# Kernel optimization log

Measured on AMD Instinct MI355X. Metric: run time of the kernel, lower is better.

## Reference

```python
import jax, jax.numpy as jnp
import numpy as np

B_, L_, D_ = 2, 1024, 2048
E_, N_, R_, K_ = 4096, 16, 128, 4
EPS = 1e-5


def setup_inputs() -> dict:
    key = jax.random.key(0)
    ks = jax.random.split(key, 12)
    s = lambda i, shape, scale=0.02: jax.random.normal(ks[i], shape, jnp.float32) * scale
    # dt bias init as in the module: inv_dt = dt + log(-expm1(-dt)), dt ~ logU[1e-3, 0.1]
    dt = jnp.exp(jax.random.uniform(ks[10], (E_,)) * (np.log(0.1) - np.log(0.001)) + np.log(0.001))
    inv_dt = dt + jnp.log(-jnp.expm1(-dt))
    return {
        'resid': jax.random.normal(ks[0], (B_, L_, D_), jnp.float32),
        'norm_w': jnp.ones((D_,), jnp.float32),
        'skip_w': s(1, (E_, D_)),
        'in_w': s(2, (E_, D_)),
        'conv_w': s(3, (E_, K_), 0.2),
        'conv_b': jnp.zeros((E_,), jnp.float32),
        'wd1': s(4, (R_, E_)),
        'wd2': s(5, (E_, R_), R_ ** -0.5),
        'wd2_b': inv_dt,
        'wB': s(6, (N_, E_)),
        'wC': s(7, (N_, E_)),
        'A_log': jnp.log(jnp.broadcast_to(jnp.arange(1, N_ + 1, dtype=jnp.float32), (E_, N_))),
        'W_D': jnp.ones((E_,), jnp.float32),
        'out_w': s(8, (D_, E_)),
    }


def _forward(resid, norm_w, skip_w, in_w, conv_w, conv_b, wd1, wd2, wd2_b,
             wB, wC, A_log, W_D, out_w):
    B, L, D = resid.shape
    E, K = conv_w.shape
    N = A_log.shape[1]
    # RMSNorm
    rn = resid * jax.lax.rsqrt(jnp.mean(resid * resid, -1, keepdims=True) + EPS) * norm_w
    skip = rn @ skip_w.T                       # [B,L,E] gate branch (z)
    x_in = rn @ in_w.T                         # [B,L,E]
    # depthwise causal conv1d (pad left K-1, truncate to L), then SiLU
    xp = jnp.pad(x_in, ((0, 0), (K - 1, 0), (0, 0)))
    conv = conv_b + sum(xp[:, k:k + L, :] * conv_w[:, k] for k in range(K))
    x = jax.nn.silu(conv)                      # [B,L,E] ssm input
    # low-rank delta, input-dependent B/C
    delta = jax.nn.softplus((x @ wd1.T) @ wd2.T + wd2_b)   # [B,L,E]
    A = -jnp.exp(A_log)                        # [E,N]
    Bm = x @ wB.T                              # [B,L,N]
    Cm = x @ wC.T                              # [B,L,N]

    def step(h, inp):
        d_l, b_l, c_l, x_l = inp               # [B,E],[B,N],[B,N],[B,E]
        h = jnp.exp(d_l[:, :, None] * A) * h + (d_l * x_l)[:, :, None] * b_l[:, None, :]
        y_l = jnp.einsum('ben,bn->be', h, c_l)
        return h, y_l

    h0 = jnp.zeros((B, E, N), resid.dtype)
    xs = (delta.transpose(1, 0, 2), Bm.transpose(1, 0, 2),
          Cm.transpose(1, 0, 2), x.transpose(1, 0, 2))
    _, ys = jax.lax.scan(step, h0, xs)         # ys: [L,B,E]
    y = ys.transpose(1, 0, 2) + x * W_D        # skip connection via D
    y = y * jax.nn.silu(skip)                  # gating
    return resid + y @ out_w.T                 # out_proj + residual


def reference(resid, norm_w, skip_w, in_w, conv_w, conv_b, wd1, wd2, wd2_b,
              wB, wC, A_log, W_D, out_w):
    return _forward(resid, norm_w, skip_w, in_w, conv_w, conv_b, wd1, wd2,
                    wd2_b, wB, wC, A_log, W_D, out_w)
```

## Files before the change

### kernel.cpp

```cpp
#include <hip/hip_runtime.h>
#include <stdint.h>

#define NB 2
#define NL 1024
#define ND 2048
#define NE 4096
#define NN 16
#define NR 128
#define NKC 4
#define NBL (NB*NL)
#define EPSV 1e-5f

typedef __attribute__((ext_vector_type(4))) float f32x4;
typedef __attribute__((ext_vector_type(8))) short short8;
typedef __attribute__((ext_vector_type(8))) unsigned short ushort8;
typedef __attribute__((ext_vector_type(4))) unsigned short ushort4_t;

__device__ __forceinline__ unsigned short f2bf(float f) {
  union { float f; unsigned u; } v; v.f = f;
  unsigned r = v.u + 0x7FFFu + ((v.u >> 16) & 1u);
  return (unsigned short)(r >> 16);
}

__device__ __forceinline__ float bf2f(unsigned short u) {
  union { unsigned u; float f; } v; v.u = (unsigned)u << 16; return v.f;
}

__device__ __forceinline__ void load_lds16(const void* g, void* l) {
  __builtin_amdgcn_global_load_lds((const __attribute__((address_space(1))) void*)g,
                                   (__attribute__((address_space(3))) void*)l,
                                   16, 0, 0);
}

template<int CTRL>
__device__ __forceinline__ float dpp_mov(float v) {
  return __int_as_float(__builtin_amdgcn_update_dpp(
      0, __float_as_int(v), CTRL, 0xF, 0xF, true));
}

__global__ void rmsnorm_kernel(const float* __restrict__ resid,
                               const float* __restrict__ nw,
                               unsigned short* __restrict__ rn) {
  int row = blockIdx.x;
  int tid = threadIdx.x;
  const float* r = resid + (size_t)row * ND;
  f32x4 v0 = *(const f32x4*)(r + tid * 8);
  f32x4 v1 = *(const f32x4*)(r + tid * 8 + 4);
  float vals[8];
#pragma unroll
  for (int i = 0; i < 4; ++i) { vals[i] = v0[i]; vals[4 + i] = v1[i]; }
  float ss = 0.f;
#pragma unroll
  for (int i = 0; i < 8; ++i) ss += vals[i] * vals[i];
  for (int o = 32; o > 0; o >>= 1) ss += __shfl_down(ss, o);
  __shared__ float ps[4];
  if ((tid & 63) == 0) ps[tid >> 6] = ss;
  __syncthreads();
  float tot = ps[0] + ps[1] + ps[2] + ps[3];
  float scale = rsqrtf(tot / (float)ND + EPSV);
  ushort8 o8;
#pragma unroll
  for (int i = 0; i < 8; ++i) o8[i] = f2bf(vals[i] * scale * nw[tid * 8 + i]);
  *(ushort8*)(rn + (size_t)row * ND + tid * 8) = o8;
}

__global__ void cast_bf16_kernel(const float* __restrict__ in,
                                 unsigned short* __restrict__ out, int n8) {
  int i = blockIdx.x * blockDim.x + threadIdx.x;
  if (i >= n8) return;
  f32x4 a = *(const f32x4*)(in + (size_t)i * 8);
  f32x4 b = *(const f32x4*)(in + (size_t)i * 8 + 4);
  ushort8 o;
#pragma unroll
  for (int j = 0; j < 4; ++j) { o[j] = f2bf(a[j]); o[4 + j] = f2bf(b[j]); }
  *(ushort8*)(out + (size_t)i * 8) = o;
}

__global__ void build_wcat_kernel(const float* __restrict__ wd1,
                                  const float* __restrict__ wB,
                                  const float* __restrict__ wC,
                                  unsigned short* __restrict__ out) {
  int i = blockIdx.x * blockDim.x + threadIdx.x;
  if (i >= 256 * NE / 8) return;
  int col8 = i & (NE / 8 - 1);
  int row = i >> 9;
  const float* src = nullptr; int srow = 0;
  if (row < 128)      { src = wd1; srow = row; }
  else if (row < 144) { src = wB;  srow = row - 128; }
  else if (row < 160) { src = wC;  srow = row - 144; }
  ushort8 o;
  if (src) {
    f32x4 a = *(const f32x4*)(src + (size_t)srow * NE + col8 * 8);
    f32x4 b = *(const f32x4*)(src + (size_t)srow * NE + col8 * 8 + 4);
#pragma unroll
    for (int j = 0; j < 4; ++j) { o[j] = f2bf(a[j]); o[4 + j] = f2bf(b[j]); }
  } else {
#pragma unroll
    for (int j = 0; j < 8; ++j) o[j] = 0;
  }
  *(ushort8*)(out + (size_t)row * NE + col8 * 8) = o;
}

__global__ __launch_bounds__(512, 2)
void gemm256_fused(const unsigned short* __restrict__ A,
                   const unsigned short* __restrict__ B,
                   float* __restrict__ Gout,
                   unsigned short* __restrict__ Xout) {
  const int K = 2048, NH = K / 32;
  __shared__ unsigned short Asl[4][8192];
  __shared__ unsigned short Bsl[4][8192];
  int tid = threadIdx.x;
  int w = tid >> 6, lane = tid & 63;
  int wm = w >> 2, wn = w & 3;
  int lr = lane & 15, kg8 = (lane >> 4) * 8;
  int m0 = blockIdx.y * 256, n0 = blockIdx.x * 256;

  const unsigned short* ga = A + (size_t)(m0 + (tid >> 2)) * K + (tid & 3) * 8;
  const unsigned short* gb = B + (size_t)(n0 + (tid >> 2)) * K + (tid & 3) * 8;
  char* ldsA0 = (char*)&Asl[0][0] + w * 1024;
  char* ldsB0 = (char*)&Bsl[0][0] + w * 1024;

  auto stageA = [&](int h) {
    int slot = h & 3, k0 = h * 32;
    load_lds16(ga + k0, ldsA0 + slot * 16384);
    load_lds16(ga + k0 + (size_t)128 * K, ldsA0 + slot * 16384 + 8192);
  };
  auto stageB = [&](int h) {
    int slot = h & 3, k0 = h * 32;
    load_lds16(gb + k0, ldsB0 + slot * 16384);
    load_lds16(gb + k0 + (size_t)128 * K, ldsB0 + slot * 16384 + 8192);
  };

  f32x4 acc[8][4];
#pragma unroll
  for (int i = 0; i < 8; ++i)
#pragma unroll
    for (int j = 0; j < 4; ++j) acc[i][j] = (f32x4){0.f, 0.f, 0.f, 0.f};

  stageA(0); stageB(0); stageA(1); stageB(1); stageA(2); stageB(2);
  asm volatile("s_waitcnt vmcnt(8)" ::: "memory");
  __builtin_amdgcn_s_barrier();

  for (int h = 0; h < NH; ++h) {
    int slot = h & 3;
    const unsigned short* As_ = &Asl[slot][0];
    const unsigned short* Bs_ = &Bsl[slot][0];
    int arow = wm * 128 + lr;
    int brow = wn * 64 + lr;
    short8 a[8], b[4];
#pragma unroll
    for (int i = 0; i < 4; ++i)
      a[i] = *(const short8*)&As_[(arow + i * 16) * 32 + kg8];
#pragma unroll
    for (int j = 0; j < 4; ++j)
      b[j] = *(const short8*)&Bs_[(brow + j * 16) * 32 + kg8];
    if (h + 3 < NH) stageA(h + 3);
    __builtin_amdgcn_s_barrier();
    __builtin_amdgcn_s_setprio(1);
#pragma unroll
    for (int i = 0; i < 4; ++i)
#pragma unroll
      for (int j = 0; j < 4; ++j)
        acc[i][j] = __builtin_amdgcn_mfma_f32_16x16x32_bf16(a[i], b[j], acc[i][j], 0, 0, 0);
    __builtin_amdgcn_s_setprio(0);
    __builtin_amdgcn_s_barrier();
#pragma unroll
    for (int i = 0; i < 4; ++i)
      a[4 + i] = *(const short8*)&As_[(arow + (4 + i) * 16) * 32 + kg8];
    if (h + 3 < NH) stageB(h + 3);
    __builtin_amdgcn_s_barrier();
    __builtin_amdgcn_s_setprio(1);
#pragma unroll
    for (int i = 0; i < 4; ++i)
#pragma unroll
      for (int j = 0; j < 4; ++j)
        acc[4 + i][j] = __builtin_amdgcn_mfma_f32_16x16x32_bf16(a[4 + i], b[j], acc[4 + i][j], 0, 0, 0);
    __builtin_amdgcn_s_setprio(0);
    if (h < NH - 3)       { asm volatile("s_waitcnt vmcnt(8)" ::: "memory"); }
    else if (h == NH - 3) { asm volatile("s_waitcnt vmcnt(4)" ::: "memory"); }
    else if (h == NH - 2) { asm volatile("s_waitcnt vmcnt(0)" ::: "memory"); }
    __builtin_amdgcn_s_barrier();
  }

  int rbase = m0 + wm * 128 + (lane >> 4) * 4;
  int cbase = n0 + wn * 64 + (lane & 15);
  bool isg = (n0 < 4096);
#pragma unroll
  for (int mf = 0; mf < 8; ++mf) {
#pragma unroll
    for (int nf = 0; nf < 4; ++nf) {
      int col = cbase + nf * 16;
#pragma unroll
      for (int rr = 0; rr < 4; ++rr) {
        int row = rbase + mf * 16 + rr;
        float v = acc[mf][nf][rr];
        if (isg) Gout[(size_t)row * 4096 + col] = v / (1.f + __expf(-v));
        else     Xout[(size_t)row * 4096 + (col - 4096)] = f2bf(v);
      }
    }
  }
}

template<int MODE>
__global__ __launch_bounds__(256)
void gemm_bt(const unsigned short* __restrict__ A,
             const unsigned short* __restrict__ B,
             float* __restrict__ C,
             int M, int N, int K, int ksteps_per_z,
             const float* __restrict__ bias,
             const float* __restrict__ add) {
  __shared__ unsigned short As[128 * 32];
  __shared__ unsigned short Bs[128 * 32];
  int tid = threadIdx.x;
  int w = tid >> 6, lane = tid & 63;
  int m0 = blockIdx.y * 128, n0 = blockIdx.x * 128;
  int kz0 = blockIdx.z * ksteps_per_z * 32;
  if (MODE == 0) C += (size_t)blockIdx.z * M * N;

  f32x4 zero = {0.f, 0.f, 0.f, 0.f};
  f32x4 acc[4][4];
#pragma unroll
  for (int i = 0; i < 4; ++i)
#pragma unroll
    for (int j = 0; j < 4; ++j) acc[i][j] = zero;

  int wm = w >> 1, wn = w & 1;
  int lr = lane & 15, kg = lane >> 4;

  int fe0 = (w)*512 + lane * 8;
  int fe1 = (4 + w) * 512 + lane * 8;
  int r0 = fe0 >> 5, c0 = fe0 & 31;
  int r1 = fe1 >> 5, c1 = fe1 & 31;
  const unsigned short* Ag0 = A + (size_t)(m0 + r0) * K + c0;
  const unsigned short* Ag1 = A + (size_t)(m0 + r1) * K + c1;
  const unsigned short* Bg0 = B + (size_t)(n0 + r0) * K + c0;
  const unsigned short* Bg1 = B + (size_t)(n0 + r1) * K + c1;
  unsigned short* Al0 = As + (w) * 512;
  unsigned short* Al1 = As + (4 + w) * 512;
  unsigned short* Bl0 = Bs + (w) * 512;
  unsigned short* Bl1 = Bs + (4 + w) * 512;

  for (int ks = 0; ks < ksteps_per_z; ++ks) {
    int kk = kz0 + ks * 32;
    __syncthreads();
    load_lds16(Ag0 + kk, Al0);
    load_lds16(Ag1 + kk, Al1);
    load_lds16(Bg0 + kk, Bl0);
    load_lds16(Bg1 + kk, Bl1);
    asm volatile("s_waitcnt vmcnt(0)" ::: "memory");
    __syncthreads();
    short8 a[4], b[4];
#pragma unroll
    for (int i = 0; i < 4; ++i)
      a[i] = *(const short8*)&As[(wm * 64 + i * 16 + lr) * 32 + kg * 8];
#pragma unroll
    for (int j = 0; j < 4; ++j)
      b[j] = *(const short8*)&Bs[(wn * 64 + j * 16 + lr) * 32 + kg * 8];
#pragma unroll
    for (int i = 0; i < 4; ++i)
#pragma unroll
      for (int j = 0; j < 4; ++j)
        acc[i][j] = __builtin_amdgcn_mfma_f32_16x16x32_bf16(a[i], b[j], acc[i][j], 0, 0, 0);
  }

#pragma unroll
  for (int i = 0; i < 4; ++i) {
#pragma unroll
    for (int j = 0; j < 4; ++j) {
      int rbase = m0 + wm * 64 + i * 16 + kg * 4;
      int col = n0 + wn * 64 + j * 16 + lr;
#pragma unroll
      for (int r = 0; r < 4; ++r) {
        float v = acc[i][j][r];
        size_t idx = (size_t)(rbase + r) * N + col;
        if (MODE == 0) {
          C[idx] = v;
        } else if (MODE == 1) {
          float t = v + bias[col];
          ((unsigned short*)C)[idx] = f2bf((t > 20.f) ? t : log1pf(__expf(t)));
        } else {
          C[idx] = v + add[idx];
        }
      }
    }
  }
}

__global__ void conv_silu_kernel(const unsigned short* __restrict__ xin,
                                 const float* __restrict__ cw,
                                 const float* __restrict__ cb,
                                 unsigned short* __restrict__ xbf) {
  size_t idx = (size_t)blockIdx.x * blockDim.x + threadIdx.x;
  if (idx >= (size_t)NB * NL * NE) return;
  int e = (int)(idx & (NE - 1));
  int r = (int)(idx >> 12);
  int l = r & (NL - 1);
  float acc = cb[e];
#pragma unroll
  for (int k = 0; k < NKC; ++k) {
    int ls = l - 3 + k;
    if (ls >= 0) acc += bf2f(xin[(size_t)(r - 3 + k) * NE + e]) * cw[e * 4 + k];
  }
  float s = acc / (1.f + __expf(-acc));
  xbf[idx] = f2bf(s);
}

__global__ void reduce_tcat_kernel(const float* __restrict__ part,
                                   unsigned short* __restrict__ tbf,
                                   float* __restrict__ bc) {
  int idx = blockIdx.x * blockDim.x + threadIdx.x;
  if (idx >= NBL * 160) return;
  int m = idx / 160, c = idx - m * 160;
  float s = 0.f;
#pragma unroll
  for (int z = 0; z < 8; ++z) s += part[(size_t)z * NBL * 256 + (size_t)m * 256 + c];
  if (c < 128) tbf[m * 128 + c] = f2bf(s);
  else if (c < 144) bc[m * 32 + (c - 128)] = s;
  else bc[m * 32 + 16 + (c - 144)] = s;
}

#define SCAN_T 64
__global__ __launch_bounds__(256)
void scan_kernel(const unsigned short* __restrict__ delta_bf,
                 const unsigned short* __restrict__ x_bf,
                 const float* __restrict__ bc,
                 const float* __restrict__ gf,
                 const float* __restrict__ A_log,
                 const float* __restrict__ W_D,
                 unsigned short* __restrict__ yg) {
  __shared__ unsigned short dxl[2][SCAN_T][2][16];
  __shared__ float gl[2][SCAN_T][16];
  __shared__ float BCl[2][SCAN_T][32];
  __shared__ float yl[SCAN_T][16];
  int tid = threadIdx.x;
  int n = tid & 15, el = tid >> 4;
  int w = tid >> 6, lane = tid & 63;
  int e0 = blockIdx.x * 16;
  int b = blockIdx.y;
  int e = e0 + el;
  float A2 = -__expf(A_log[e * 16 + n]) * 1.44269504f;
  float wd = W_D[e];
  float h = 0.f;

  const unsigned short* gdl = delta_bf + (size_t)b * NL * NE + e0;
  const unsigned short* gx  = x_bf + (size_t)b * NL * NE + e0;
  const float* gg  = gf + (size_t)b * NL * 4096 + e0;
  const float* gBC = bc + (size_t)b * NL * 32;

  const unsigned short* dxsrc = ((lane >> 1) & 1) ? gx : gdl;
  int dxrow = w * 16 + (lane >> 2);
  int dxcol = (lane & 1) * 8;
  int grow = w * 16 + (lane >> 2);
  int gcol = (lane & 3) * 4;
  int bcrow = lane >> 3;
  int bccol = (lane & 7) * 4;

  auto stage = [&](int buf, int c) {
    int l0 = c * SCAN_T;
    load_lds16(dxsrc + (size_t)(l0 + dxrow) * NE + dxcol, &dxl[buf][w * 16][0][0]);
    load_lds16(gg + (size_t)(l0 + grow) * 4096 + gcol, &gl[buf][w * 16][0]);
    load_lds16(gBC + (size_t)(l0 + w * 16 + bcrow) * 32 + bccol, &BCl[buf][w * 16][0]);
    load_lds16(gBC + (size_t)(l0 + w * 16 + 8 + bcrow) * 32 + bccol, &BCl[buf][w * 16 + 8][0]);
  };

  stage(0, 0);
  const int nch = NL / SCAN_T;
  for (int c = 0; c < nch; ++c) {
    int cur = c & 1;
    if (c + 1 < nch) {
      stage(cur ^ 1, c + 1);
      asm volatile("s_waitcnt vmcnt(4)" ::: "memory");
    } else {
      asm volatile("s_waitcnt vmcnt(0)" ::: "memory");
    }
    __syncthreads();
    int l0 = c * SCAN_T;
#pragma unroll 8
    for (int t = 0; t < SCAN_T; ++t) {
      float dc = bf2f(dxl[cur][t][0][el]);
      float xc = bf2f(dxl[cur][t][1][el]);
      float Bc = BCl[cur][t][n];
      float Cc = BCl[cur][t][16 + n];
      float a = dc * A2, ed;
      asm("v_exp_f32 %0, %1" : "=v"(ed) : "v"(a));
      h = ed * h + (dc * xc) * Bc;
      float p = h * Cc;
      p += dpp_mov<0xB1>(p);
      p += dpp_mov<0x4E>(p);
      p += dpp_mov<0x141>(p);
      p += dpp_mov<0x140>(p);
      if (n == 0) yl[t][el] = p + xc * wd;
    }
    __syncthreads();
    {
      int t = tid >> 2, part = tid & 3;
      f32x4 yv = *(const f32x4*)&yl[t][part * 4];
      f32x4 gv = *(const f32x4*)&gl[cur][t][part * 4];
      ushort4_t o;
#pragma unroll
      for (int j = 0; j < 4; ++j) o[j] = f2bf(yv[j] * gv[j]);
      *(ushort4_t*)(yg + (size_t)(b * NL + l0 + t) * NE + e0 + part * 4) = o;
    }
    __syncthreads();
  }
}

extern "C" void kernel_launch(void* const* d_in, const int* in_sizes, int n_in,
                              void* d_out, int out_size, void* d_ws, size_t ws_size,
                              hipStream_t stream) {
  const float* resid  = (const float*)d_in[0];
  const float* norm_w = (const float*)d_in[1];
  const float* skip_w = (const float*)d_in[2];
  const float* in_w   = (const float*)d_in[3];
  const float* conv_w = (const float*)d_in[4];
  const float* conv_b = (const float*)d_in[5];
  const float* wd1    = (const float*)d_in[6];
  const float* wd2    = (const float*)d_in[7];
  const float* wd2_b  = (const float*)d_in[8];
  const float* wB     = (const float*)d_in[9];
  const float* wC     = (const float*)d_in[10];
  const float* A_log  = (const float*)d_in[11];
  const float* W_D    = (const float*)d_in[12];
  const float* out_w  = (const float*)d_in[13];
  float* out = (float*)d_out;

  char* ws = (char*)d_ws;
  size_t off = 0;
  auto alloc = [&](size_t bytes) -> void* {
    void* p = ws + off;
    off += (bytes + 255) & ~(size_t)255;
    return p;
  };
  unsigned short* rn_bf      = (unsigned short*)alloc((size_t)NBL * ND * 2);
  unsigned short* wskipin_bf = (unsigned short*)alloc((size_t)2 * NE * ND * 2);
  unsigned short* wout_bf    = (unsigned short*)alloc((size_t)ND * NE * 2);
  unsigned short* wd2_bf     = (unsigned short*)alloc((size_t)NE * NR * 2);
  unsigned short* wcat_bf    = (unsigned short*)alloc((size_t)256 * NE * 2);
  float* g_f                 = (float*)alloc((size_t)NBL * NE * 4);
  unsigned short* xin_bf     = (unsigned short*)alloc((size_t)NBL * NE * 2);
  unsigned short* x_bf       = (unsigned short*)alloc((size_t)NBL * NE * 2);
  float* part_f              = (float*)alloc((size_t)8 * NBL * 256 * 4);
  unsigned short* t_bf       = (unsigned short*)alloc((size_t)NBL * NR * 2);
  float* bc_f                = (float*)alloc((size_t)NBL * 32 * 4);
  unsigned short* yg_bf      = (unsigned short*)alloc((size_t)NBL * NE * 2);
  unsigned short* delta_bf = wskipin_bf;
  (void)ws_size; (void)in_sizes; (void)n_in; (void)out_size;

  rmsnorm_kernel<<<dim3(NBL), dim3(256), 0, stream>>>(resid, norm_w, rn_bf);

  cast_bf16_kernel<<<dim3((NE * ND / 8 + 255) / 256), dim3(256), 0, stream>>>(skip_w, wskipin_bf, NE * ND / 8);
  cast_bf16_kernel<<<dim3((NE * ND / 8 + 255) / 256), dim3(256), 0, stream>>>(in_w, wskipin_bf + (size_t)NE * ND, NE * ND / 8);
  cast_bf16_kernel<<<dim3((ND * NE / 8 + 255) / 256), dim3(256), 0, stream>>>(out_w, wout_bf, ND * NE / 8);
  cast_bf16_kernel<<<dim3((NE * NR / 8 + 255) / 256), dim3(256), 0, stream>>>(wd2, wd2_bf, NE * NR / 8);
  build_wcat_kernel<<<dim3(256 * NE / 8 / 256), dim3(256), 0, stream>>>(wd1, wB, wC, wcat_bf);

  gemm256_fused<<<dim3(8192 / 256, NBL / 256), dim3(512), 0, stream>>>(
      rn_bf, wskipin_bf, g_f, xin_bf);

  conv_silu_kernel<<<dim3((int)(((size_t)NB * NL * NE) / 256)), dim3(256), 0, stream>>>(
      xin_bf, conv_w, conv_b, x_bf);

  gemm_bt<0><<<dim3(256 / 128, NBL / 128, 8), dim3(256), 0, stream>>>(
      x_bf, wcat_bf, part_f, NBL, 256, NE, (NE / 32) / 8, nullptr, nullptr);
  reduce_tcat_kernel<<<dim3((NBL * 160 + 255) / 256), dim3(256), 0, stream>>>(
      part_f, t_bf, bc_f);

  gemm_bt<1><<<dim3(NE / 128, NBL / 128, 1), dim3(256), 0, stream>>>(
      t_bf, wd2_bf, (float*)delta_bf, NBL, NE, NR, NR / 32, wd2_b, nullptr);

  scan_kernel<<<dim3(NE / 16, NB), dim3(256), 0, stream>>>(
      delta_bf, x_bf, bc_f, g_f, A_log, W_D, yg_bf);

  gemm_bt<2><<<dim3(ND / 128, NBL / 128, 1), dim3(256), 0, stream>>>(
      yg_bf, wout_bf, out, NBL, ND, NE, NE / 32, nullptr, resid);
}
```

Measured before the change: 426.8 us.

## Split selective scan into four sequence segments with a carry-correction pass

The sequential scan over L is split into four 256-step segments, each run from zero state in parallel (grid grows from 512 to 2048 blocks). Each segment writes its final state and summed delta. A second kernel then propagates the carried state into segments 1-3, adds the correction term exp(A*cumdelta)*h*C to the stored partial y, and applies the gate. The aim is to expose more parallelism on a latency-bound recurrence. The cost is an extra kernel and a read-modify-write of yg for three quarters of the sequence, with intermediate y rounded to bf16 before the correction is added.

```diff
diff --git a/kernel.cpp b/kernel.cpp
--- a/kernel.cpp
+++ b/kernel.cpp
@@ -10,6 +10,8 @@
 #define NKC 4
 #define NBL (NB*NL)
 #define EPSV 1e-5f
+#define SEG_T 256
+#define SCAN_T 64
 
 typedef __attribute__((ext_vector_type(4))) float f32x4;
 typedef __attribute__((ext_vector_type(8))) short short8;
@@ -319,28 +321,30 @@
   else bc[m * 32 + 16 + (c - 144)] = s;
 }
 
-#define SCAN_T 64
 __global__ __launch_bounds__(256)
-void scan_kernel(const unsigned short* __restrict__ delta_bf,
-                 const unsigned short* __restrict__ x_bf,
-                 const float* __restrict__ bc,
-                 const float* __restrict__ gf,
-                 const float* __restrict__ A_log,
-                 const float* __restrict__ W_D,
-                 unsigned short* __restrict__ yg) {
+void scan1_kernel(const unsigned short* __restrict__ delta_bf,
+                  const unsigned short* __restrict__ x_bf,
+                  const float* __restrict__ bc,
+                  const float* __restrict__ gf,
+                  const float* __restrict__ A_log,
+                  const float* __restrict__ W_D,
+                  unsigned short* __restrict__ yg,
+                  float* __restrict__ fin,
+                  float* __restrict__ dtot) {
   __shared__ unsigned short dxl[2][SCAN_T][2][16];
   __shared__ float gl[2][SCAN_T][16];
   __shared__ float BCl[2][SCAN_T][32];
-  __shared__ float yl[SCAN_T][16];
+  __shared__ float yl2[SCAN_T][16][2];
+  __shared__ float wdl[16];
   int tid = threadIdx.x;
   int n = tid & 15, el = tid >> 4;
   int w = tid >> 6, lane = tid & 63;
   int e0 = blockIdx.x * 16;
-  int b = blockIdx.y;
+  int b = blockIdx.y >> 2, seg = blockIdx.y & 3;
   int e = e0 + el;
   float A2 = -__expf(A_log[e * 16 + n]) * 1.44269504f;
-  float wd = W_D[e];
-  float h = 0.f;
+  if (tid < 16) wdl[tid] = W_D[e0 + tid];
+  float h = 0.f, cum = 0.f;
 
   const unsigned short* gdl = delta_bf + (size_t)b * NL * NE + e0;
   const unsigned short* gx  = x_bf + (size_t)b * NL * NE + e0;
@@ -356,31 +360,35 @@
   int bccol = (lane & 7) * 4;
 
   auto stage = [&](int buf, int c) {
-    int l0 = c * SCAN_T;
+    int l0 = seg * SEG_T + c * SCAN_T;
     load_lds16(dxsrc + (size_t)(l0 + dxrow) * NE + dxcol, &dxl[buf][w * 16][0][0]);
-    load_lds16(gg + (size_t)(l0 + grow) * 4096 + gcol, &gl[buf][w * 16][0]);
+    if (seg == 0)
+      load_lds16(gg + (size_t)(l0 + grow) * 4096 + gcol, &gl[buf][w * 16][0]);
     load_lds16(gBC + (size_t)(l0 + w * 16 + bcrow) * 32 + bccol, &BCl[buf][w * 16][0]);
     load_lds16(gBC + (size_t)(l0 + w * 16 + 8 + bcrow) * 32 + bccol, &BCl[buf][w * 16 + 8][0]);
   };
 
   stage(0, 0);
-  const int nch = NL / SCAN_T;
+  const int nch = SEG_T / SCAN_T;
   for (int c = 0; c < nch; ++c) {
     int cur = c & 1;
     if (c + 1 < nch) {
       stage(cur ^ 1, c + 1);
-      asm volatile("s_waitcnt vmcnt(4)" ::: "memory");
+      if (seg == 0) { asm volatile("s_waitcnt vmcnt(4)" ::: "memory"); }
+      else          { asm volatile("s_waitcnt vmcnt(3)" ::: "memory"); }
     } else {
       asm volatile("s_waitcnt vmcnt(0)" ::: "memory");
     }
     __syncthreads();
-    int l0 = c * SCAN_T;
+    const unsigned short (*dxc)[2][16] = dxl[cur];
+    const float (*BCc)[32] = BCl[cur];
 #pragma unroll 8
     for (int t = 0; t < SCAN_T; ++t) {
-      float dc = bf2f(dxl[cur][t][0][el]);
-      float xc = bf2f(dxl[cur][t][1][el]);
-      float Bc = BCl[cur][t][n];
-      float Cc = BCl[cur][t][16 + n];
+      float dc = bf2f(dxc[t][0][el]);
+      float xc = bf2f(dxc[t][1][el]);
+      float Bc = BCc[t][n];
+      float Cc = BCc[t][16 + n];
+      cum += dc;
       float a = dc * A2, ed;
       asm("v_exp_f32 %0, %1" : "=v"(ed) : "v"(a));
       h = ed * h + (dc * xc) * Bc;
@@ -388,18 +396,115 @@
       p += dpp_mov<0xB1>(p);
       p += dpp_mov<0x4E>(p);
       p += dpp_mov<0x141>(p);
-      p += dpp_mov<0x140>(p);
-      if (n == 0) yl[t][el] = p + xc * wd;
+      if ((n & 7) == 0) yl2[t][el][n >> 3] = p;
     }
     __syncthreads();
     {
       int t = tid >> 2, part = tid & 3;
-      f32x4 yv = *(const f32x4*)&yl[t][part * 4];
-      f32x4 gv = *(const f32x4*)&gl[cur][t][part * 4];
+      int l0 = seg * SEG_T + c * SCAN_T;
       ushort4_t o;
 #pragma unroll
-      for (int j = 0; j < 4; ++j) o[j] = f2bf(yv[j] * gv[j]);
+      for (int j = 0; j < 4; ++j) {
+        int ee = part * 4 + j;
+        float xv = bf2f(dxc[t][1][ee]);
+        float y = yl2[t][ee][0] + yl2[t][ee][1] + xv * wdl[ee];
+        if (seg == 0) y *= gl[cur][t][ee];
+        o[j] = f2bf(y);
+      }
       *(ushort4_t*)(yg + (size_t)(b * NL + l0 + t) * NE + e0 + part * 4) = o;
+    }
+    __syncthreads();
+  }
+  fin[(size_t)((seg * 2 + b) * 4096 + e) * 16 + n] = h;
+  if (n == 0) dtot[(size_t)(seg * 2 + b) * 4096 + e] = cum;
+}
+
+__global__ __launch_bounds__(256)
+void scan2_kernel(const unsigned short* __restrict__ delta_bf,
+                  unsigned short* __restrict__ yg,
+                  const float* __restrict__ bc,
+                  const float* __restrict__ gf,
+                  const float* __restrict__ A_log,
+                  const float* __restrict__ fin,
+                  const float* __restrict__ dtot) {
+  __shared__ unsigned short dl[2][SCAN_T][16];
+  __shared__ unsigned short ypl[2][SCAN_T][16];
+  __shared__ float Cl[2][SCAN_T][16];
+  __shared__ float gl2[2][SCAN_T][16];
+  __shared__ float ycl[SCAN_T][16][2];
+  int tid = threadIdx.x;
+  int n = tid & 15, el = tid >> 4;
+  int w = tid >> 6, lane = tid & 63;
+  int e0 = blockIdx.x * 16;
+  int b = blockIdx.y / 3, seg = 1 + blockIdx.y % 3;
+  int e = e0 + el;
+  float A2 = -__expf(A_log[e * 16 + n]) * 1.44269504f;
+  float h = fin[(size_t)(b * 4096 + e) * 16 + n];
+  for (int s2 = 1; s2 < seg; ++s2) {
+    float dt = dtot[(size_t)(s2 * 2 + b) * 4096 + e];
+    float a = A2 * dt, pw;
+    asm("v_exp_f32 %0, %1" : "=v"(pw) : "v"(a));
+    h = fin[(size_t)((s2 * 2 + b) * 4096 + e) * 16 + n] + pw * h;
+  }
+
+  const unsigned short* gd = delta_bf + (size_t)b * NL * NE + e0;
+  unsigned short* gy = yg + (size_t)b * NL * NE + e0;
+  const float* gg  = gf + (size_t)b * NL * 4096 + e0;
+  const float* gBC = bc + (size_t)b * NL * 32;
+
+  int crow = w * 16 + (lane >> 2);
+  int ccol = 16 + (lane & 3) * 4;
+  int grow = w * 16 + (lane >> 2);
+  int gcol = (lane & 3) * 4;
+  int dyrow = (w & 1) * 32 + (lane >> 1);
+  int dycol = (lane & 1) * 8;
+
+  auto stage = [&](int buf, int c) {
+    int l0 = seg * SEG_T + c * SCAN_T;
+    load_lds16(gBC + (size_t)(l0 + crow) * 32 + ccol, &Cl[buf][w * 16][0]);
+    load_lds16(gg + (size_t)(l0 + grow) * 4096 + gcol, &gl2[buf][w * 16][0]);
+    if (w < 2) load_lds16(gd + (size_t)(l0 + dyrow) * NE + dycol, &dl[buf][(w & 1) * 32][0]);
+    else       load_lds16(gy + (size_t)(l0 + dyrow) * NE + dycol, &ypl[buf][(w & 1) * 32][0]);
+  };
+
+  stage(0, 0);
+  float cum = 0.f;
+  const int nch = SEG_T / SCAN_T;
+  for (int c = 0; c < nch; ++c) {
+    int cur = c & 1;
+    if (c + 1 < nch) {
+      stage(cur ^ 1, c + 1);
+      asm volatile("s_waitcnt vmcnt(3)" ::: "memory");
+    } else {
+      asm volatile("s_waitcnt vmcnt(0)" ::: "memory");
+    }
+    __syncthreads();
+    const unsigned short (*dc_)[16] = dl[cur];
+    const float (*Cc_)[16] = Cl[cur];
+#pragma unroll 8
+    for (int t = 0; t < SCAN_T; ++t) {
+      float dcv = bf2f(dc_[t][el]);
+      cum += dcv;
+      float a = A2 * cum, pw;
+      asm("v_exp_f32 %0, %1" : "=v"(pw) : "v"(a));
+      float p = (pw * h) * Cc_[t][n];
+      p += dpp_mov<0xB1>(p);
+      p += dpp_mov<0x4E>(p);
+      p += dpp_mov<0x141>(p);
+      if ((n & 7) == 0) ycl[t][el][n >> 3] = p;
+    }
+    __syncthreads();
+    {
+      int t = tid >> 2, part = tid & 3;
+      int l0 = seg * SEG_T + c * SCAN_T;
+      ushort4_t o;
+#pragma unroll
+      for (int j = 0; j < 4; ++j) {
+        int ee = part * 4 + j;
+        float y = ycl[t][ee][0] + ycl[t][ee][1] + bf2f(ypl[cur][t][ee]);
+        o[j] = f2bf(y * gl2[cur][t][ee]);
+      }
+      *(ushort4_t*)(gy + (size_t)(l0 + t) * NE + part * 4) = o;
     }
     __syncthreads();
   }
@@ -443,6 +548,8 @@
   unsigned short* t_bf       = (unsigned short*)alloc((size_t)NBL * NR * 2);
   float* bc_f                = (float*)alloc((size_t)NBL * 32 * 4);
   unsigned short* yg_bf      = (unsigned short*)alloc((size_t)NBL * NE * 2);
+  float* fin_f               = (float*)alloc((size_t)4 * NB * NE * 16 * 4);
+  float* dtot_f              = (float*)alloc((size_t)4 * NB * NE * 4);
   unsigned short* delta_bf = wskipin_bf;
   (void)ws_size; (void)in_sizes; (void)n_in; (void)out_size;
 
@@ -468,8 +575,10 @@
   gemm_bt<1><<<dim3(NE / 128, NBL / 128, 1), dim3(256), 0, stream>>>(
       t_bf, wd2_bf, (float*)delta_bf, NBL, NE, NR, NR / 32, wd2_b, nullptr);
 
-  scan_kernel<<<dim3(NE / 16, NB), dim3(256), 0, stream>>>(
-      delta_bf, x_bf, bc_f, g_f, A_log, W_D, yg_bf);
+  scan1_kernel<<<dim3(NE / 16, NB * 4), dim3(256), 0, stream>>>(
+      delta_bf, x_bf, bc_f, g_f, A_log, W_D, yg_bf, fin_f, dtot_f);
+  scan2_kernel<<<dim3(NE / 16, NB * 3), dim3(256), 0, stream>>>(
+      delta_bf, yg_bf, bc_f, g_f, A_log, fin_f, dtot_f);
 
   gemm_bt<2><<<dim3(ND / 128, NBL / 128, 1), dim3(256), 0, stream>>>(
       yg_bf, wout_bf, out, NBL, ND, NE, NE / 32, nullptr, resid);
```

Result: slower. 463.2 us (+8.5%).
